# Kernel optimization log

Measured on AMD Instinct MI355X. Metric: run time of the kernel, lower is better.

## Reference

```python
import jax, jax.numpy as jnp
import numpy as np

N, E = 50000, 640000
DIN, DH, DOUT = 128, 256, 128


def _glorot(k, i, o):
    return jax.random.normal(k, (i, o), jnp.float32) / np.sqrt(i)


def setup_inputs() -> dict:
    key = jax.random.key(0)
    ks = jax.random.split(key, 12)
    return {
        "x": jax.random.normal(ks[0], (N, DIN), jnp.float32),
        "edge_index": jax.random.randint(ks[1], (2, E), 0, N, dtype=jnp.int32),
        # SAGEConv 1: in -> hidden (lin_l on aggregated w/ bias, lin_r on root)
        "W1l": _glorot(ks[2], DIN, DH), "b1l": jnp.zeros((DH,), jnp.float32), "W1r": _glorot(ks[3], DIN, DH),
        "g1": jnp.ones((DH,), jnp.float32), "be1": jnp.zeros((DH,), jnp.float32),
        # skip projection (in != hidden)
        "Wsk": _glorot(ks[4], DIN, DH), "bsk": jnp.zeros((DH,), jnp.float32),
        # SAGEConv 2: hidden -> hidden
        "W2l": _glorot(ks[5], DH, DH), "b2l": jnp.zeros((DH,), jnp.float32), "W2r": _glorot(ks[6], DH, DH),
        "g2": jnp.ones((DH,), jnp.float32), "be2": jnp.zeros((DH,), jnp.float32),
        # SAGEConv 3: hidden -> out
        "W3l": _glorot(ks[7], DH, DOUT), "b3l": jnp.zeros((DOUT,), jnp.float32), "W3r": _glorot(ks[8], DH, DOUT),
    }


def _sage_conv(x, src, dst, Wl, bl, Wr, n):
    # mean aggregation of source features into destination nodes
    msg = x[src]                                                 # [E, d]
    agg = jax.ops.segment_sum(msg, dst, num_segments=n)          # [N, d]
    cnt = jax.ops.segment_sum(jnp.ones((src.shape[0],), x.dtype), dst, num_segments=n)
    agg = agg / jnp.maximum(cnt, 1.0)[:, None]
    return agg @ Wl + bl + x @ Wr


def _layernorm(x, g, b):
    mu = jnp.mean(x, axis=-1, keepdims=True)
    var = jnp.mean((x - mu) ** 2, axis=-1, keepdims=True)
    return (x - mu) * jax.lax.rsqrt(var + 1e-5) * g + b


def reference(x, edge_index, W1l, b1l, W1r, g1, be1, Wsk, bsk,
              W2l, b2l, W2r, g2, be2, W3l, b3l, W3r):
    src, dst = edge_index[0], edge_index[1]
    n = x.shape[0]
    # layer 0: conv -> LN -> relu -> (dropout p=0, eval) -> skip via projection
    h = _sage_conv(x, src, dst, W1l, b1l, W1r, n)
    h = jax.nn.relu(_layernorm(h, g1, be1))
    h = h + (x @ Wsk + bsk)
    # layer 1: conv -> LN -> relu -> residual add (shapes match)
    h2 = _sage_conv(h, src, dst, W2l, b2l, W2r, n)
    h2 = jax.nn.relu(_layernorm(h2, g2, be2)) + h
    # final conv (no norm/act)
    return _sage_conv(h2, src, dst, W3l, b3l, W3r, n)
```

## Files before the change

kernel.cpp:

```cpp
#include <hip/hip_runtime.h>


typedef float floatx4 __attribute__((ext_vector_type(4)));
typedef float floatx2 __attribute__((ext_vector_type(2)));
typedef short bf16x8 __attribute__((ext_vector_type(8)));

__device__ inline unsigned short f2bf(float f) {
    unsigned u = __float_as_uint(f);
    unsigned r = (u + 0x7fffu + ((u >> 16) & 1u)) >> 16;
    return (unsigned short)r;
}
__device__ inline float bf2f_lo(unsigned v) { return __uint_as_float(v << 16); }
__device__ inline float bf2f_hi(unsigned v) { return __uint_as_float(v & 0xffff0000u); }

__device__ inline void gl_lds16(const void* g, void* l) {
    __builtin_amdgcn_global_load_lds((const __attribute__((address_space(1))) unsigned int*)g,
                                     (__attribute__((address_space(3))) unsigned int*)l,
                                     16, 0, 0);
}

__global__ void hist_kernel(const int* __restrict__ dst, int* __restrict__ cnt, int E) {
    int i = blockIdx.x * blockDim.x + threadIdx.x;
    if (i < E) atomicAdd(&cnt[dst[i]], 1);
}

#define SCAN_CHUNK 2048

__global__ __launch_bounds__(256) void scan_blocksums(const int* __restrict__ cnt,
                                                      int* __restrict__ bsum, int N) {
    __shared__ int sh[256];
    int t = threadIdx.x;
    int base = blockIdx.x * SCAN_CHUNK + t * 8;
    int s = 0;
#pragma unroll
    for (int i = 0; i < 8; i++) {
        int idx = base + i;
        if (idx < N) s += cnt[idx];
    }
    sh[t] = s;
    __syncthreads();
    for (int off = 1; off < 256; off <<= 1) {
        int v = (t >= off) ? sh[t - off] : 0;
        __syncthreads();
        sh[t] += v;
        __syncthreads();
    }
    if (t == 255) bsum[blockIdx.x] = sh[255];
}

__global__ __launch_bounds__(256) void scan_bsums(const int* __restrict__ bsum,
                                                  int* __restrict__ boff, int NB,
                                                  int* __restrict__ rowptr, int N, int E) {
    __shared__ int sh[256];
    int t = threadIdx.x;
    int v = (t < NB) ? bsum[t] : 0;
    sh[t] = v;
    __syncthreads();
    for (int off = 1; off < 256; off <<= 1) {
        int u = (t >= off) ? sh[t - off] : 0;
        __syncthreads();
        sh[t] += u;
        __syncthreads();
    }
    if (t < NB) boff[t] = sh[t] - v;
    if (t == 0) rowptr[N] = E;
}

__global__ __launch_bounds__(256) void scan_final(const int* __restrict__ cnt,
                                                  const int* __restrict__ boff,
                                                  int* __restrict__ rowptr,
                                                  int* __restrict__ cursor,
                                                  float* __restrict__ invdeg, int N) {
    __shared__ int sh[256];
    int t = threadIdx.x;
    int base = blockIdx.x * SCAN_CHUNK + t * 8;
    int c[8];
    int s = 0;
#pragma unroll
    for (int i = 0; i < 8; i++) {
        int idx = base + i;
        c[i] = (idx < N) ? cnt[idx] : 0;
        s += c[i];
    }
    sh[t] = s;
    __syncthreads();
    for (int off = 1; off < 256; off <<= 1) {
        int v = (t >= off) ? sh[t - off] : 0;
        __syncthreads();
        sh[t] += v;
        __syncthreads();
    }
    int run = boff[blockIdx.x] + sh[t] - s;
#pragma unroll
    for (int i = 0; i < 8; i++) {
        int idx = base + i;
        if (idx < N) {
            rowptr[idx] = run;
            cursor[idx] = run;
            invdeg[idx] = 1.0f / (float)(c[i] > 1 ? c[i] : 1);
            run += c[i];
        }
    }
}

__global__ void scatter_kernel(const int* __restrict__ src, const int* __restrict__ dst,
                               int* __restrict__ cursor, int* __restrict__ col, int E) {
    int i = blockIdx.x * blockDim.x + threadIdx.x;
    if (i < E) {
        int p = atomicAdd(&cursor[dst[i]], 1);
        col[p] = src[i];
    }
}

__global__ void prep_weights(const float* __restrict__ W1l, const float* __restrict__ W1r,
                             const float* __restrict__ Wsk, const float* __restrict__ W2l,
                             const float* __restrict__ W2r, const float* __restrict__ W3l,
                             const float* __restrict__ W3r, const float* __restrict__ b1l,
                             const float* __restrict__ bsk,
                             unsigned short* __restrict__ WtC, unsigned short* __restrict__ Wt2,
                             unsigned short* __restrict__ Wt3, float* __restrict__ biasC) {
    int i = blockIdx.x * blockDim.x + threadIdx.x;
    if (i < 32768) {
        int k = i >> 8, n = i & 255;
        WtC[n * 256 + k] = f2bf(W1l[i]);
    } else if (i < 65536) {
        int j = i - 32768, k = j >> 8, n = j & 255;
        WtC[n * 256 + 128 + k] = f2bf(W1r[j]);
    } else if (i < 98304) {
        int j = i - 65536, k = j >> 8, n = j & 255;
        WtC[(256 + n) * 256 + 128 + k] = f2bf(Wsk[j]);
    } else if (i < 131072) {
        int j = i - 98304, k = j >> 8, n = j & 255;
        WtC[(256 + n) * 256 + k] = 0;
    } else if (i < 196608) {
        int j = i - 131072, k = j >> 8, n = j & 255;
        Wt2[n * 512 + k] = f2bf(W2l[j]);
    } else if (i < 262144) {
        int j = i - 196608, k = j >> 8, n = j & 255;
        Wt2[n * 512 + 256 + k] = f2bf(W2r[j]);
    } else if (i < 294912) {
        int j = i - 262144, k = j >> 7, n = j & 127;
        Wt3[n * 256 + k] = f2bf(W3l[j]);
    } else if (i < 327680) {
        int j = i - 294912, k = j >> 7, n = j & 127;
        Wt3[(128 + n) * 256 + k] = f2bf(W3r[j]);
    } else if (i < 328192) {
        int j = i - 327680;
        biasC[j] = (j < 256) ? b1l[j] : bsk[j - 256];
    }
}

__global__ void cvt_x2(const float* __restrict__ x, unsigned short* __restrict__ A1cat,
                       unsigned char* __restrict__ X8, int total32) {
    int i = blockIdx.x * blockDim.x + threadIdx.x;
    if (i >= total32) return;
    int r = i >> 5, c4 = (i & 31) * 4;
    float4 v = *(const float4*)(x + (size_t)r * 128 + c4);
    ushort4 o;
    o.x = f2bf(v.x); o.y = f2bf(v.y); o.z = f2bf(v.z); o.w = f2bf(v.w);
    *(ushort4*)(A1cat + (size_t)r * 256 + 128 + c4) = o;
    unsigned wpk = 0;
    wpk = __builtin_amdgcn_cvt_pk_fp8_f32(v.x, v.y, wpk, false);
    wpk = __builtin_amdgcn_cvt_pk_fp8_f32(v.z, v.w, wpk, true);
    *(unsigned*)(X8 + (size_t)r * 128 + c4) = wpk;
}

__device__ inline void acc16_fp8(uint4 v, float m, floatx2* a) {
    floatx2 mm = {m, m};
    floatx2 p;
    p = __builtin_amdgcn_cvt_pk_f32_fp8(v.x, false); a[0] = p * mm + a[0];
    p = __builtin_amdgcn_cvt_pk_f32_fp8(v.x, true);  a[1] = p * mm + a[1];
    p = __builtin_amdgcn_cvt_pk_f32_fp8(v.y, false); a[2] = p * mm + a[2];
    p = __builtin_amdgcn_cvt_pk_f32_fp8(v.y, true);  a[3] = p * mm + a[3];
    p = __builtin_amdgcn_cvt_pk_f32_fp8(v.z, false); a[4] = p * mm + a[4];
    p = __builtin_amdgcn_cvt_pk_f32_fp8(v.z, true);  a[5] = p * mm + a[5];
    p = __builtin_amdgcn_cvt_pk_f32_fp8(v.w, false); a[6] = p * mm + a[6];
    p = __builtin_amdgcn_cvt_pk_f32_fp8(v.w, true);  a[7] = p * mm + a[7];
}

__device__ inline void acc8_bf16(uint4 v, float m, floatx2* a) {
    floatx2 mm = {m, m};
    floatx2 p;
    p = (floatx2){bf2f_lo(v.x), bf2f_hi(v.x)}; a[0] = p * mm + a[0];
    p = (floatx2){bf2f_lo(v.y), bf2f_hi(v.y)}; a[1] = p * mm + a[1];
    p = (floatx2){bf2f_lo(v.z), bf2f_hi(v.z)}; a[2] = p * mm + a[2];
    p = (floatx2){bf2f_lo(v.w), bf2f_hi(v.w)}; a[3] = p * mm + a[3];
}

template <int RSB>
__global__ __launch_bounds__(256) void agg_fp8_g(const int* __restrict__ rowptr,
                                                 const int* __restrict__ col,
                                                 const float* __restrict__ invdeg,
                                                 const unsigned char* __restrict__ T8,
                                                 unsigned short* __restrict__ out, int ostride, int N) {
    constexpr int LPR = RSB / 16;
    constexpr int NPW = 64 / LPR;
    int wid = (blockIdx.x * blockDim.x + threadIdx.x) >> 6;
    int lane = threadIdx.x & 63;
    int sub = lane & (LPR - 1);
    int g = lane / LPR;
    int node = wid * NPW + g;
    bool vn = node < N;
    int nc = vn ? node : N - 1;
    int s = rowptr[nc];
    int e = vn ? rowptr[nc + 1] : s;
    const unsigned char* To = T8 + sub * 16;
    floatx2 a[8];
#pragma unroll
    for (int i = 0; i < 8; i++) a[i] = (floatx2){0.f, 0.f};
    for (int j = s; j < e; j += 8) {
        int j1 = (j + 1 < e) ? j + 1 : j;
        int j2 = (j + 2 < e) ? j + 2 : j;
        int j3 = (j + 3 < e) ? j + 3 : j;
        int j4 = (j + 4 < e) ? j + 4 : j;
        int j5 = (j + 5 < e) ? j + 5 : j;
        int j6 = (j + 6 < e) ? j + 6 : j;
        int j7 = (j + 7 < e) ? j + 7 : j;
        float m1 = (j + 1 < e) ? 1.f : 0.f;
        float m2 = (j + 2 < e) ? 1.f : 0.f;
        float m3 = (j + 3 < e) ? 1.f : 0.f;
        float m4 = (j + 4 < e) ? 1.f : 0.f;
        float m5 = (j + 5 < e) ? 1.f : 0.f;
        float m6 = (j + 6 < e) ? 1.f : 0.f;
        float m7 = (j + 7 < e) ? 1.f : 0.f;
        int c0 = col[j], c1 = col[j1], c2 = col[j2], c3 = col[j3];
        int c4 = col[j4], c5 = col[j5], c6 = col[j6], c7 = col[j7];
        uint4 v0 = *(const uint4*)(To + (size_t)c0 * RSB);
        uint4 v1 = *(const uint4*)(To + (size_t)c1 * RSB);
        uint4 v2 = *(const uint4*)(To + (size_t)c2 * RSB);
        uint4 v3 = *(const uint4*)(To + (size_t)c3 * RSB);
        uint4 v4 = *(const uint4*)(To + (size_t)c4 * RSB);
        uint4 v5 = *(const uint4*)(To + (size_t)c5 * RSB);
        uint4 v6 = *(const uint4*)(To + (size_t)c6 * RSB);
        uint4 v7 = *(const uint4*)(To + (size_t)c7 * RSB);
        acc16_fp8(v0, 1.f, a);
        acc16_fp8(v1, m1, a);
        acc16_fp8(v2, m2, a);
        acc16_fp8(v3, m3, a);
        acc16_fp8(v4, m4, a);
        acc16_fp8(v5, m5, a);
        acc16_fp8(v6, m6, a);
        acc16_fp8(v7, m7, a);
    }
    if (vn) {
        float inv = invdeg[node];
        uint4 o1, o2;
        o1.x = (unsigned)f2bf(a[0].x * inv) | ((unsigned)f2bf(a[0].y * inv) << 16);
        o1.y = (unsigned)f2bf(a[1].x * inv) | ((unsigned)f2bf(a[1].y * inv) << 16);
        o1.z = (unsigned)f2bf(a[2].x * inv) | ((unsigned)f2bf(a[2].y * inv) << 16);
        o1.w = (unsigned)f2bf(a[3].x * inv) | ((unsigned)f2bf(a[3].y * inv) << 16);
        o2.x = (unsigned)f2bf(a[4].x * inv) | ((unsigned)f2bf(a[4].y * inv) << 16);
        o2.y = (unsigned)f2bf(a[5].x * inv) | ((unsigned)f2bf(a[5].y * inv) << 16);
        o2.z = (unsigned)f2bf(a[6].x * inv) | ((unsigned)f2bf(a[6].y * inv) << 16);
        o2.w = (unsigned)f2bf(a[7].x * inv) | ((unsigned)f2bf(a[7].y * inv) << 16);
        unsigned short* op = out + (size_t)node * ostride + sub * 16;
        *(uint4*)op = o1;
        *(uint4*)(op + 8) = o2;
    }
}

__global__ __launch_bounds__(256) void agg_fin_g(const int* __restrict__ rowptr,
                                                 const int* __restrict__ col,
                                                 const float* __restrict__ invdeg,
                                                 const unsigned short* __restrict__ T,
                                                 const float* __restrict__ R,
                                                 float* __restrict__ out, int N) {
    int wid = (blockIdx.x * blockDim.x + threadIdx.x) >> 6;
    int lane = threadIdx.x & 63;
    int sub = lane & 15;
    int g = lane >> 4;
    int node = wid * 4 + g;
    bool vn = node < N;
    int nc = vn ? node : N - 1;
    int s = rowptr[nc];
    int e = vn ? rowptr[nc + 1] : s;
    const unsigned short* To = T + sub * 8;
    floatx2 a[4];
#pragma unroll
    for (int i = 0; i < 4; i++) a[i] = (floatx2){0.f, 0.f};
    for (int j = s; j < e; j += 8) {
        int j1 = (j + 1 < e) ? j + 1 : j;
        int j2 = (j + 2 < e) ? j + 2 : j;
        int j3 = (j + 3 < e) ? j + 3 : j;
        int j4 = (j + 4 < e) ? j + 4 : j;
        int j5 = (j + 5 < e) ? j + 5 : j;
        int j6 = (j + 6 < e) ? j + 6 : j;
        int j7 = (j + 7 < e) ? j + 7 : j;
        float m1 = (j + 1 < e) ? 1.f : 0.f;
        float m2 = (j + 2 < e) ? 1.f : 0.f;
        float m3 = (j + 3 < e) ? 1.f : 0.f;
        float m4 = (j + 4 < e) ? 1.f : 0.f;
        float m5 = (j + 5 < e) ? 1.f : 0.f;
        float m6 = (j + 6 < e) ? 1.f : 0.f;
        float m7 = (j + 7 < e) ? 1.f : 0.f;
        int c0 = col[j], c1 = col[j1], c2 = col[j2], c3 = col[j3];
        int c4 = col[j4], c5 = col[j5], c6 = col[j6], c7 = col[j7];
        uint4 v0 = *(const uint4*)(To + (size_t)c0 * 128);
        uint4 v1 = *(const uint4*)(To + (size_t)c1 * 128);
        uint4 v2 = *(const uint4*)(To + (size_t)c2 * 128);
        uint4 v3 = *(const uint4*)(To + (size_t)c3 * 128);
        uint4 v4 = *(const uint4*)(To + (size_t)c4 * 128);
        uint4 v5 = *(const uint4*)(To + (size_t)c5 * 128);
        uint4 v6 = *(const uint4*)(To + (size_t)c6 * 128);
        uint4 v7 = *(const uint4*)(To + (size_t)c7 * 128);
        acc8_bf16(v0, 1.f, a);
        acc8_bf16(v1, m1, a);
        acc8_bf16(v2, m2, a);
        acc8_bf16(v3, m3, a);
        acc8_bf16(v4, m4, a);
        acc8_bf16(v5, m5, a);
        acc8_bf16(v6, m6, a);
        acc8_bf16(v7, m7, a);
    }
    if (vn) {
        float inv = invdeg[node];
        const float* Rp = R + (size_t)node * 128 + sub * 8;
        float4 r1 = *(const float4*)Rp;
        float4 r2 = *(const float4*)(Rp + 4);
        float4 o1, o2;
        o1.x = a[0].x * inv + r1.x; o1.y = a[0].y * inv + r1.y;
        o1.z = a[1].x * inv + r1.z; o1.w = a[1].y * inv + r1.w;
        o2.x = a[2].x * inv + r2.x; o2.y = a[2].y * inv + r2.y;
        o2.z = a[3].x * inv + r2.z; o2.w = a[3].y * inv + r2.w;
        float* op = out + (size_t)node * 128 + sub * 8;
        *(float4*)op = o1;
        *(float4*)(op + 4) = o2;
    }
}

template <int KIT2, int NPAN, int MODE>
__global__ __launch_bounds__(512) void gemm_fused(
    const unsigned short* __restrict__ A, int lda,
    const unsigned short* __restrict__ B, int ldb,
    const float* __restrict__ bias,
    const float* __restrict__ gamma, const float* __restrict__ beta,
    const unsigned short* __restrict__ resid,
    unsigned short* __restrict__ outb,
    unsigned char* __restrict__ h8,
    float* __restrict__ outf, int M) {
    constexpr int COLS = NPAN * 256;
    constexpr int LNW = COLS + 8;
    constexpr int STAGE_E = 128 * 128;
    constexpr int DBUF_F = 2 * STAGE_E / 2;
    constexpr int SMEM_F = (DBUF_F > 32 * LNW) ? DBUF_F : 32 * LNW;
    __shared__ __align__(16) float smemf[SMEM_F];
    unsigned short* sbase = (unsigned short*)smemf;

    int t = threadIdx.x;
    int lane = t & 63, w = t >> 6;
    int bm = blockIdx.x * 128;
    int wm = (w & 1) * 64, wn = (w >> 1) * 64;
    int m16 = lane & 15, kq = lane >> 4;
    const int fsw = m16 & 7;

    floatx4 acc[NPAN][4][4];
#pragma unroll
    for (int p = 0; p < NPAN; p++)
#pragma unroll
        for (int i = 0; i < 4; i++)
#pragma unroll
            for (int j = 0; j < 4; j++) acc[p][i][j] = (floatx4){0.f, 0.f, 0.f, 0.f};

    auto stage = [&](int kt, int bsel) {
        unsigned short* s = sbase + bsel * STAGE_E;
        int k0 = kt * 128;
#pragma unroll
        for (int i = 0; i < 4; i++) {
            int gs = i * 512 + t;
            int kh = gs >> 10;
            int ls = gs & 1023;
            int row = ls >> 3, j = ls & 7;
            int kc = j ^ (row & 7);
            int rowA = bm + row;
            if (rowA > M - 1) rowA = M - 1;
            gl_lds16(A + (size_t)rowA * lda + k0 + kh * 64 + kc * 8, (void*)&s[(size_t)gs * 8]);
        }
    };

    stage(0, 0);
    __syncthreads();
    for (int kt = 0; kt < KIT2; kt++) {
        if (kt + 1 < KIT2) stage(kt + 1, (kt & 1) ^ 1);
        const unsigned short* sA = sbase + (kt & 1) * STAGE_E;
#pragma unroll
        for (int kh = 0; kh < 2; kh++) {
            const unsigned short* sT = sA + kh * 8192;
#pragma unroll
            for (int ks = 0; ks < 2; ks++) {
                int kcl = (ks << 2) | kq;
                bf16x8 af[4];
#pragma unroll
                for (int mi = 0; mi < 4; mi++)
                    af[mi] = *(const bf16x8*)&sT[(wm + mi * 16 + m16) * 64 + ((kcl ^ fsw)) * 8];
#pragma unroll
                for (int p = 0; p < NPAN; p++) {
                    if (MODE == 0 && p == 1 && kt == 0) continue;
                    const unsigned short* Bp = B + (size_t)(wn + p * 256) * ldb + kt * 128 + kh * 64;
                    bf16x8 bf[4];
#pragma unroll
                    for (int ni = 0; ni < 4; ni++)
                        bf[ni] = *(const bf16x8*)&Bp[(size_t)(ni * 16 + m16) * ldb + kcl * 8];
#pragma unroll
                    for (int mi = 0; mi < 4; mi++)
#pragma unroll
                        for (int ni = 0; ni < 4; ni++)
                            acc[p][mi][ni] =
                                __builtin_amdgcn_mfma_f32_16x16x32_bf16(af[mi], bf[ni], acc[p][mi][ni], 0, 0, 0);
                }
            }
        }
        __syncthreads();
    }

    float* lnb = smemf;
    int c4 = lane * 4;
    float4 bu = {0.f, 0.f, 0.f, 0.f}, bs = {0.f, 0.f, 0.f, 0.f};
    float4 gv = {0.f, 0.f, 0.f, 0.f}, bv = {0.f, 0.f, 0.f, 0.f};
    float4 b3 = {0.f, 0.f, 0.f, 0.f};
    if (MODE == 0) {
        bu = *(const float4*)&bias[c4];
        bs = *(const float4*)&bias[256 + c4];
        gv = *(const float4*)&gamma[c4];
        bv = *(const float4*)&beta[c4];
    } else if (MODE == 1) {
        bu = *(const float4*)&bias[c4];
        gv = *(const float4*)&gamma[c4];
        bv = *(const float4*)&beta[c4];
    } else {
        if (lane >= 32) b3 = *(const float4*)&bias[c4 - 128];
    }

#pragma unroll
    for (int g4 = 0; g4 < 4; g4++) {
        if (wm == (g4 >> 1) * 64) {
            int mi0 = (g4 & 1) * 2;
#pragma unroll
            for (int p = 0; p < NPAN; p++)
#pragma unroll
                for (int mm = 0; mm < 2; mm++)
#pragma unroll
                    for (int ni = 0; ni < 4; ni++)
#pragma unroll
                        for (int r = 0; r < 4; r++)
                            lnb[(mm * 16 + kq * 4 + r) * LNW + wn + p * 256 + ni * 16 + m16] =
                                acc[p][mi0 + mm][ni][r];
        }
        __syncthreads();
#pragma unroll
        for (int rr = 0; rr < 4; rr++) {
            int lrow = w * 4 + rr;
            int grow = bm + g4 * 32 + lrow;
            bool valid = grow < M;
            float4 u = *(const float4*)&lnb[lrow * LNW + c4];
            if (MODE <= 1) {
                u.x += bu.x; u.y += bu.y; u.z += bu.z; u.w += bu.w;
                float s1 = (u.x + u.y) + (u.z + u.w);
                float s2 = (u.x * u.x + u.y * u.y) + (u.z * u.z + u.w * u.w);
#pragma unroll
                for (int off = 1; off < 64; off <<= 1) {
                    s1 += __shfl_xor(s1, off, 64);
                    s2 += __shfl_xor(s2, off, 64);
                }
                float mu = s1 * (1.f / 256.f);
                float var = s2 * (1.f / 256.f) - mu * mu;
                float rs = rsqrtf(var + 1e-5f);
                float a0, a1, a2, a3;
                if (MODE == 0) {
                    float4 sv = *(const float4*)&lnb[lrow * LNW + 256 + c4];
                    a0 = sv.x + bs.x; a1 = sv.y + bs.y; a2 = sv.z + bs.z; a3 = sv.w + bs.w;
                } else {
                    int gr = valid ? grow : M - 1;
                    uint2 hv = *(const uint2*)(resid + (size_t)gr * 512 + c4);
                    a0 = bf2f_lo(hv.x); a1 = bf2f_hi(hv.x); a2 = bf2f_lo(hv.y); a3 = bf2f_hi(hv.y);
                }
                float o0 = fmaxf((u.x - mu) * rs * gv.x + bv.x, 0.f) + a0;
                float o1 = fmaxf((u.y - mu) * rs * gv.y + bv.y, 0.f) + a1;
                float o2 = fmaxf((u.z - mu) * rs * gv.z + bv.z, 0.f) + a2;
                float o3 = fmaxf((u.w - mu) * rs * gv.w + bv.w, 0.f) + a3;
                if (valid) {
                    ushort4 o;
                    o.x = f2bf(o0); o.y = f2bf(o1); o.z = f2bf(o2); o.w = f2bf(o3);
                    *(ushort4*)(outb + (size_t)grow * 512 + c4) = o;
                    if (MODE == 0) {
                        unsigned wpk = 0;
                        wpk = __builtin_amdgcn_cvt_pk_fp8_f32(o0, o1, wpk, false);
                        wpk = __builtin_amdgcn_cvt_pk_fp8_f32(o2, o3, wpk, true);
                        *(unsigned*)(h8 + (size_t)grow * 256 + c4) = wpk;
                    }
                }
            } else {
                if (valid) {
                    if (lane < 32) {
                        ushort4 o;
                        o.x = f2bf(u.x); o.y = f2bf(u.y); o.z = f2bf(u.z); o.w = f2bf(u.w);
                        *(ushort4*)(outb + (size_t)grow * 128 + c4) = o;
                    } else {
                        float4 o;
                        o.x = u.x + b3.x; o.y = u.y + b3.y; o.z = u.z + b3.z; o.w = u.w + b3.w;
                        *(float4*)(outf + (size_t)grow * 128 + (c4 - 128)) = o;
                    }
                }
            }
        }
        __syncthreads();
    }
}

extern "C" void kernel_launch(void* const* d_in, const int* in_sizes, int n_in,
                              void* d_out, int out_size, void* d_ws, size_t ws_size,
                              hipStream_t stream) {
    const float* x   = (const float*)d_in[0];
    const int*   ei  = (const int*)d_in[1];
    const float* W1l = (const float*)d_in[2];
    const float* b1l = (const float*)d_in[3];
    const float* W1r = (const float*)d_in[4];
    const float* g1  = (const float*)d_in[5];
    const float* be1 = (const float*)d_in[6];
    const float* Wsk = (const float*)d_in[7];
    const float* bsk = (const float*)d_in[8];
    const float* W2l = (const float*)d_in[9];
    const float* b2l = (const float*)d_in[10];
    const float* W2r = (const float*)d_in[11];
    const float* g2  = (const float*)d_in[12];
    const float* be2 = (const float*)d_in[13];
    const float* W3l = (const float*)d_in[14];
    const float* b3l = (const float*)d_in[15];
    const float* W3r = (const float*)d_in[16];

    const int N = in_sizes[0] / 128;
    const int E = in_sizes[1] / 2;
    const int* src = ei;
    const int* dst = ei + E;

    char* p = (char*)d_ws;
    auto alloc = [&](size_t bytes) {
        void* r = (void*)p;
        p += (bytes + 255) & ~(size_t)255;
        return r;
    };
    int*   cnt    = (int*)alloc(sizeof(int) * N);
    int*   rowptr = (int*)alloc(sizeof(int) * (N + 1));
    int*   cursor = (int*)alloc(sizeof(int) * N);
    float* invdeg = (float*)alloc(sizeof(float) * N);
    int*   col    = (int*)alloc(sizeof(int) * E);
    int*   bsum   = (int*)alloc(sizeof(int) * 256);
    int*   boff   = (int*)alloc(sizeof(int) * 256);
    unsigned short* A1cat = (unsigned short*)alloc(sizeof(short) * (size_t)N * 256);
    unsigned short* A2cat = (unsigned short*)alloc(sizeof(short) * (size_t)N * 512);
    float* r3 = (float*)alloc(sizeof(float) * (size_t)N * 128);
    unsigned char* H8 = (unsigned char*)alloc((size_t)N * 256);
    unsigned char* X8 = (unsigned char*)alloc((size_t)N * 128);
    unsigned short* WtC = (unsigned short*)alloc(sizeof(short) * 512 * 256);
    unsigned short* Wt2 = (unsigned short*)alloc(sizeof(short) * 256 * 512);
    unsigned short* Wt3 = (unsigned short*)alloc(sizeof(short) * 256 * 256);
    float* biasC = (float*)alloc(sizeof(float) * 512);
    unsigned short* t3 = A1cat;

    hipMemsetAsync(cnt, 0, sizeof(int) * N, stream);
    hist_kernel<<<(E + 255) / 256, 256, 0, stream>>>(dst, cnt, E);
    int NB = (N + SCAN_CHUNK - 1) / SCAN_CHUNK;
    scan_blocksums<<<NB, 256, 0, stream>>>(cnt, bsum, N);
    scan_bsums<<<1, 256, 0, stream>>>(bsum, boff, NB, rowptr, N, E);
    scan_final<<<NB, 256, 0, stream>>>(cnt, boff, rowptr, cursor, invdeg, N);
    scatter_kernel<<<(E + 255) / 256, 256, 0, stream>>>(src, dst, cursor, col, E);

    prep_weights<<<(328192 + 255) / 256, 256, 0, stream>>>(W1l, W1r, Wsk, W2l, W2r, W3l, W3r,
                                                           b1l, bsk, WtC, Wt2, Wt3, biasC);
    cvt_x2<<<((N * 32) + 255) / 256, 256, 0, stream>>>(x, A1cat, X8, N * 32);

    int mBlocks = (N + 127) / 128;
    int agg1Blocks = (N + 31) / 32;
    int agg2Blocks = (N + 15) / 16;
    int aggFBlocks = (N + 15) / 16;

    agg_fp8_g<128><<<agg1Blocks, 256, 0, stream>>>(rowptr, col, invdeg, X8, A1cat, 256, N);
    gemm_fused<2, 2, 0><<<mBlocks, 512, 0, stream>>>(A1cat, 256, WtC, 256, biasC, g1, be1,
                                                     nullptr, A2cat + 256, H8, nullptr, N);

    agg_fp8_g<256><<<agg2Blocks, 256, 0, stream>>>(rowptr, col, invdeg, H8, A2cat, 512, N);
    gemm_fused<4, 1, 1><<<mBlocks, 512, 0, stream>>>(A2cat, 512, Wt2, 512, b2l, g2, be2,
                                                     A2cat + 256, A2cat, nullptr, nullptr, N);

    gemm_fused<2, 1, 2><<<mBlocks, 512, 0, stream>>>(A2cat, 512, Wt3, 256, b3l, nullptr, nullptr,
                                                     nullptr, t3, nullptr, r3, N);
    agg_fin_g<<<aggFBlocks, 256, 0, stream>>>(rowptr, col, invdeg, t3, r3, (float*)d_out, N);
}
```

Before: 396.9 us.

## Fuse neighbor aggregation into the per-layer GEMM with LDS-resident operands

Replaces the separate fp8 gather-aggregate kernels for layers 1 and 2 with a fused kernel. Each 128-row block gathers and mean-aggregates neighbor features straight into swizzled LDS tiles, while the root-feature half is loaded asynchronously into LDS. The full-K MFMA GEMM with LayerNorm/ReLU/residual epilogue then runs from those tiles. This removes the global write and re-read of the aggregated bf16 matrix and two kernel launches. In exchange the block needs up to 128KB of LDS, which limits occupancy, and the irregular gather runs in a 512-thread GEMM block with less latency hiding.

```diff
diff --git a/kernel.cpp b/kernel.cpp
--- a/kernel.cpp
+++ b/kernel.cpp
@@ -187,78 +187,6 @@
     p = (floatx2){bf2f_lo(v.w), bf2f_hi(v.w)}; a[3] = p * mm + a[3];
 }
 
-template <int RSB>
-__global__ __launch_bounds__(256) void agg_fp8_g(const int* __restrict__ rowptr,
-                                                 const int* __restrict__ col,
-                                                 const float* __restrict__ invdeg,
-                                                 const unsigned char* __restrict__ T8,
-                                                 unsigned short* __restrict__ out, int ostride, int N) {
-    constexpr int LPR = RSB / 16;
-    constexpr int NPW = 64 / LPR;
-    int wid = (blockIdx.x * blockDim.x + threadIdx.x) >> 6;
-    int lane = threadIdx.x & 63;
-    int sub = lane & (LPR - 1);
-    int g = lane / LPR;
-    int node = wid * NPW + g;
-    bool vn = node < N;
-    int nc = vn ? node : N - 1;
-    int s = rowptr[nc];
-    int e = vn ? rowptr[nc + 1] : s;
-    const unsigned char* To = T8 + sub * 16;
-    floatx2 a[8];
-#pragma unroll
-    for (int i = 0; i < 8; i++) a[i] = (floatx2){0.f, 0.f};
-    for (int j = s; j < e; j += 8) {
-        int j1 = (j + 1 < e) ? j + 1 : j;
-        int j2 = (j + 2 < e) ? j + 2 : j;
-        int j3 = (j + 3 < e) ? j + 3 : j;
-        int j4 = (j + 4 < e) ? j + 4 : j;
-        int j5 = (j + 5 < e) ? j + 5 : j;
-        int j6 = (j + 6 < e) ? j + 6 : j;
-        int j7 = (j + 7 < e) ? j + 7 : j;
-        float m1 = (j + 1 < e) ? 1.f : 0.f;
-        float m2 = (j + 2 < e) ? 1.f : 0.f;
-        float m3 = (j + 3 < e) ? 1.f : 0.f;
-        float m4 = (j + 4 < e) ? 1.f : 0.f;
-        float m5 = (j + 5 < e) ? 1.f : 0.f;
-        float m6 = (j + 6 < e) ? 1.f : 0.f;
-        float m7 = (j + 7 < e) ? 1.f : 0.f;
-        int c0 = col[j], c1 = col[j1], c2 = col[j2], c3 = col[j3];
-        int c4 = col[j4], c5 = col[j5], c6 = col[j6], c7 = col[j7];
-        uint4 v0 = *(const uint4*)(To + (size_t)c0 * RSB);
-        uint4 v1 = *(const uint4*)(To + (size_t)c1 * RSB);
-        uint4 v2 = *(const uint4*)(To + (size_t)c2 * RSB);
-        uint4 v3 = *(const uint4*)(To + (size_t)c3 * RSB);
-        uint4 v4 = *(const uint4*)(To + (size_t)c4 * RSB);
-        uint4 v5 = *(const uint4*)(To + (size_t)c5 * RSB);
-        uint4 v6 = *(const uint4*)(To + (size_t)c6 * RSB);
-        uint4 v7 = *(const uint4*)(To + (size_t)c7 * RSB);
-        acc16_fp8(v0, 1.f, a);
-        acc16_fp8(v1, m1, a);
-        acc16_fp8(v2, m2, a);
-        acc16_fp8(v3, m3, a);
-        acc16_fp8(v4, m4, a);
-        acc16_fp8(v5, m5, a);
-        acc16_fp8(v6, m6, a);
-        acc16_fp8(v7, m7, a);
-    }
-    if (vn) {
-        float inv = invdeg[node];
-        uint4 o1, o2;
-        o1.x = (unsigned)f2bf(a[0].x * inv) | ((unsigned)f2bf(a[0].y * inv) << 16);
-        o1.y = (unsigned)f2bf(a[1].x * inv) | ((unsigned)f2bf(a[1].y * inv) << 16);
-        o1.z = (unsigned)f2bf(a[2].x * inv) | ((unsigned)f2bf(a[2].y * inv) << 16);
-        o1.w = (unsigned)f2bf(a[3].x * inv) | ((unsigned)f2bf(a[3].y * inv) << 16);
-        o2.x = (unsigned)f2bf(a[4].x * inv) | ((unsigned)f2bf(a[4].y * inv) << 16);
-        o2.y = (unsigned)f2bf(a[5].x * inv) | ((unsigned)f2bf(a[5].y * inv) << 16);
-        o2.z = (unsigned)f2bf(a[6].x * inv) | ((unsigned)f2bf(a[6].y * inv) << 16);
-        o2.w = (unsigned)f2bf(a[7].x * inv) | ((unsigned)f2bf(a[7].y * inv) << 16);
-        unsigned short* op = out + (size_t)node * ostride + sub * 16;
-        *(uint4*)op = o1;
-        *(uint4*)(op + 8) = o2;
-    }
-}
-
 __global__ __launch_bounds__(256) void agg_fin_g(const int* __restrict__ rowptr,
                                                  const int* __restrict__ col,
                                                  const float* __restrict__ invdeg,
@@ -328,23 +256,28 @@
     }
 }
 
-template <int KIT2, int NPAN, int MODE>
-__global__ __launch_bounds__(512) void gemm_fused(
-    const unsigned short* __restrict__ A, int lda,
+template <int MODE>
+__global__ __launch_bounds__(512) void fused_layer(
+    const int* __restrict__ rowptr, const int* __restrict__ col,
+    const float* __restrict__ invdeg,
+    const unsigned char* __restrict__ T8, int RSBc,
+    const unsigned short* __restrict__ Aright, int lda,
     const unsigned short* __restrict__ B, int ldb,
     const float* __restrict__ bias,
     const float* __restrict__ gamma, const float* __restrict__ beta,
     const unsigned short* __restrict__ resid,
     unsigned short* __restrict__ outb,
-    unsigned char* __restrict__ h8,
-    float* __restrict__ outf, int M) {
+    unsigned char* __restrict__ h8, int N) {
+    constexpr int KSUB = (MODE == 0) ? 4 : 8;
+    constexpr int GSUB = (MODE == 0) ? 2 : 4;
+    constexpr int RSUB = KSUB - GSUB;
+    constexpr int NPAN = (MODE == 0) ? 2 : 1;
     constexpr int COLS = NPAN * 256;
     constexpr int LNW = COLS + 8;
-    constexpr int STAGE_E = 128 * 128;
-    constexpr int DBUF_F = 2 * STAGE_E / 2;
-    constexpr int SMEM_F = (DBUF_F > 32 * LNW) ? DBUF_F : 32 * LNW;
+    constexpr int A_E = KSUB * 8192;
+    constexpr int SMEM_F = ((A_E / 2) > 32 * LNW) ? (A_E / 2) : 32 * LNW;
     __shared__ __align__(16) float smemf[SMEM_F];
-    unsigned short* sbase = (unsigned short*)smemf;
+    unsigned short* Ab = (unsigned short*)smemf;
 
     int t = threadIdx.x;
     int lane = t & 63, w = t >> 6;
@@ -353,6 +286,94 @@
     int m16 = lane & 15, kq = lane >> 4;
     const int fsw = m16 & 7;
 
+#pragma unroll
+    for (int i = 0; i < RSUB * 2; i++) {
+        int s = i * 512 + t;
+        int st = GSUB + (s >> 10);
+        int ls = s & 1023;
+        int row = ls >> 3, j = ls & 7;
+        int kc = j ^ (row & 7);
+        int rowA = bm + row;
+        if (rowA > N - 1) rowA = N - 1;
+        gl_lds16(Aright + (size_t)rowA * lda + (st - GSUB) * 64 + kc * 8,
+                 (void*)&Ab[(size_t)st * 8192 + (size_t)ls * 8]);
+    }
+
+    {
+        const int LPR = (MODE == 0) ? 8 : 16;
+        const int NG = 512 / LPR;
+        const int NPG = 128 / NG;
+        int sub = t & (LPR - 1);
+        int g = t / LPR;
+        const int RSB = RSBc;
+        const unsigned char* To = T8 + sub * 16;
+#pragma unroll
+        for (int i = 0; i < NPG; i++) {
+            int rl = g + i * NG;
+            int node = bm + rl;
+            bool vn = node < N;
+            int nc = vn ? node : N - 1;
+            int s = rowptr[nc];
+            int e = vn ? rowptr[nc + 1] : s;
+            floatx2 a[8];
+#pragma unroll
+            for (int q = 0; q < 8; q++) a[q] = (floatx2){0.f, 0.f};
+            for (int j = s; j < e; j += 8) {
+                int j1 = (j + 1 < e) ? j + 1 : j;
+                int j2 = (j + 2 < e) ? j + 2 : j;
+                int j3 = (j + 3 < e) ? j + 3 : j;
+                int j4 = (j + 4 < e) ? j + 4 : j;
+                int j5 = (j + 5 < e) ? j + 5 : j;
+                int j6 = (j + 6 < e) ? j + 6 : j;
+                int j7 = (j + 7 < e) ? j + 7 : j;
+                float m1 = (j + 1 < e) ? 1.f : 0.f;
+                float m2 = (j + 2 < e) ? 1.f : 0.f;
+                float m3 = (j + 3 < e) ? 1.f : 0.f;
+                float m4 = (j + 4 < e) ? 1.f : 0.f;
+                float m5 = (j + 5 < e) ? 1.f : 0.f;
+                float m6 = (j + 6 < e) ? 1.f : 0.f;
+                float m7 = (j + 7 < e) ? 1.f : 0.f;
+                int c0 = col[j], c1 = col[j1], c2 = col[j2], c3 = col[j3];
+                int c4 = col[j4], c5 = col[j5], c6 = col[j6], c7 = col[j7];
+                uint4 v0 = *(const uint4*)(To + (size_t)c0 * RSB);
+                uint4 v1 = *(const uint4*)(To + (size_t)c1 * RSB);
+                uint4 v2 = *(const uint4*)(To + (size_t)c2 * RSB);
+                uint4 v3 = *(const uint4*)(To + (size_t)c3 * RSB);
+                uint4 v4 = *(const uint4*)(To + (size_t)c4 * RSB);
+                uint4 v5 = *(const uint4*)(To + (size_t)c5 * RSB);
+                uint4 v6 = *(const uint4*)(To + (size_t)c6 * RSB);
+                uint4 v7 = *(const uint4*)(To + (size_t)c7 * RSB);
+                acc16_fp8(v0, 1.f, a);
+                acc16_fp8(v1, m1, a);
+                acc16_fp8(v2, m2, a);
+                acc16_fp8(v3, m3, a);
+                acc16_fp8(v4, m4, a);
+                acc16_fp8(v5, m5, a);
+                acc16_fp8(v6, m6, a);
+                acc16_fp8(v7, m7, a);
+            }
+            if (vn) {
+                float inv = invdeg[node];
+                uint4 o1, o2;
+                o1.x = (unsigned)f2bf(a[0].x * inv) | ((unsigned)f2bf(a[0].y * inv) << 16);
+                o1.y = (unsigned)f2bf(a[1].x * inv) | ((unsigned)f2bf(a[1].y * inv) << 16);
+                o1.z = (unsigned)f2bf(a[2].x * inv) | ((unsigned)f2bf(a[2].y * inv) << 16);
+                o1.w = (unsigned)f2bf(a[3].x * inv) | ((unsigned)f2bf(a[3].y * inv) << 16);
+                o2.x = (unsigned)f2bf(a[4].x * inv) | ((unsigned)f2bf(a[4].y * inv) << 16);
+                o2.y = (unsigned)f2bf(a[5].x * inv) | ((unsigned)f2bf(a[5].y * inv) << 16);
+                o2.z = (unsigned)f2bf(a[6].x * inv) | ((unsigned)f2bf(a[6].y * inv) << 16);
+                o2.w = (unsigned)f2bf(a[7].x * inv) | ((unsigned)f2bf(a[7].y * inv) << 16);
+                int kt = sub >> 2;
+                int c0k = (sub & 3) * 2;
+                size_t base = (size_t)kt * 8192 + (size_t)rl * 64;
+                *(uint4*)&Ab[base + (size_t)((c0k ^ (rl & 7)) * 8)] = o1;
+                *(uint4*)&Ab[base + (size_t)(((c0k + 1) ^ (rl & 7)) * 8)] = o2;
+            }
+        }
+    }
+    asm volatile("s_waitcnt vmcnt(0)" ::: "memory");
+    __syncthreads();
+
     floatx4 acc[NPAN][4][4];
 #pragma unroll
     for (int p = 0; p < NPAN; p++)
@@ -360,6 +381,139 @@
         for (int i = 0; i < 4; i++)
 #pragma unroll
             for (int j = 0; j < 4; j++) acc[p][i][j] = (floatx4){0.f, 0.f, 0.f, 0.f};
+
+#pragma unroll
+    for (int kt = 0; kt < KSUB; kt++) {
+        const unsigned short* sT = Ab + kt * 8192;
+#pragma unroll
+        for (int ks = 0; ks < 2; ks++) {
+            int kcl = (ks << 2) | kq;
+            bf16x8 af[4];
+#pragma unroll
+            for (int mi = 0; mi < 4; mi++)
+                af[mi] = *(const bf16x8*)&sT[(wm + mi * 16 + m16) * 64 + ((kcl ^ fsw)) * 8];
+#pragma unroll
+            for (int p = 0; p < NPAN; p++) {
+                if (MODE == 0 && p == 1 && kt < 2) continue;
+                const unsigned short* Bp = B + (size_t)(wn + p * 256) * ldb + kt * 64;
+                bf16x8 bf[4];
+#pragma unroll
+                for (int ni = 0; ni < 4; ni++)
+                    bf[ni] = *(const bf16x8*)&Bp[(size_t)(ni * 16 + m16) * ldb + kcl * 8];
+#pragma unroll
+                for (int mi = 0; mi < 4; mi++)
+#pragma unroll
+                    for (int ni = 0; ni < 4; ni++)
+                        acc[p][mi][ni] =
+                            __builtin_amdgcn_mfma_f32_16x16x32_bf16(af[mi], bf[ni], acc[p][mi][ni], 0, 0, 0);
+            }
+        }
+    }
+    __syncthreads();
+
+    float* lnb = smemf;
+    int c4 = lane * 4;
+    float4 bu = {0.f, 0.f, 0.f, 0.f}, bs = {0.f, 0.f, 0.f, 0.f};
+    float4 gv = {0.f, 0.f, 0.f, 0.f}, bv = {0.f, 0.f, 0.f, 0.f};
+    if (MODE == 0) {
+        bu = *(const float4*)&bias[c4];
+        bs = *(const float4*)&bias[256 + c4];
+        gv = *(const float4*)&gamma[c4];
+        bv = *(const float4*)&beta[c4];
+    } else {
+        bu = *(const float4*)&bias[c4];
+        gv = *(const float4*)&gamma[c4];
+        bv = *(const float4*)&beta[c4];
+    }
+
+#pragma unroll
+    for (int g4 = 0; g4 < 4; g4++) {
+        if (wm == (g4 >> 1) * 64) {
+            int mi0 = (g4 & 1) * 2;
+#pragma unroll
+            for (int p = 0; p < NPAN; p++)
+#pragma unroll
+                for (int mm = 0; mm < 2; mm++)
+#pragma unroll
+                    for (int ni = 0; ni < 4; ni++)
+#pragma unroll
+                        for (int r = 0; r < 4; r++)
+                            lnb[(mm * 16 + kq * 4 + r) * LNW + wn + p * 256 + ni * 16 + m16] =
+                                acc[p][mi0 + mm][ni][r];
+        }
+        __syncthreads();
+#pragma unroll
+        for (int rr = 0; rr < 4; rr++) {
+            int lrow = w * 4 + rr;
+            int grow = bm + g4 * 32 + lrow;
+            bool valid = grow < N;
+            float4 u = *(const float4*)&lnb[lrow * LNW + c4];
+            u.x += bu.x; u.y += bu.y; u.z += bu.z; u.w += bu.w;
+            float s1 = (u.x + u.y) + (u.z + u.w);
+            float s2 = (u.x * u.x + u.y * u.y) + (u.z * u.z + u.w * u.w);
+#pragma unroll
+            for (int off = 1; off < 64; off <<= 1) {
+                s1 += __shfl_xor(s1, off, 64);
+                s2 += __shfl_xor(s2, off, 64);
+            }
+            float mu = s1 * (1.f / 256.f);
+            float var = s2 * (1.f / 256.f) - mu * mu;
+            float rs = rsqrtf(var + 1e-5f);
+            float a0, a1, a2, a3;
+            if (MODE == 0) {
+                float4 sv = *(const float4*)&lnb[lrow * LNW + 256 + c4];
+                a0 = sv.x + bs.x; a1 = sv.y + bs.y; a2 = sv.z + bs.z; a3 = sv.w + bs.w;
+            } else {
+                int gr = valid ? grow : N - 1;
+                uint2 hv = *(const uint2*)(resid + (size_t)gr * 512 + c4);
+                a0 = bf2f_lo(hv.x); a1 = bf2f_hi(hv.x); a2 = bf2f_lo(hv.y); a3 = bf2f_hi(hv.y);
+            }
+            float o0 = fmaxf((u.x - mu) * rs * gv.x + bv.x, 0.f) + a0;
+            float o1 = fmaxf((u.y - mu) * rs * gv.y + bv.y, 0.f) + a1;
+            float o2 = fmaxf((u.z - mu) * rs * gv.z + bv.z, 0.f) + a2;
+            float o3 = fmaxf((u.w - mu) * rs * gv.w + bv.w, 0.f) + a3;
+            if (valid) {
+                ushort4 o;
+                o.x = f2bf(o0); o.y = f2bf(o1); o.z = f2bf(o2); o.w = f2bf(o3);
+                *(ushort4*)(outb + (size_t)grow * 512 + c4) = o;
+                if (MODE == 0) {
+                    unsigned wpk = 0;
+                    wpk = __builtin_amdgcn_cvt_pk_fp8_f32(o0, o1, wpk, false);
+                    wpk = __builtin_amdgcn_cvt_pk_fp8_f32(o2, o3, wpk, true);
+                    *(unsigned*)(h8 + (size_t)grow * 256 + c4) = wpk;
+                }
+            }
+        }
+        __syncthreads();
+    }
+}
+
+template <int KIT2>
+__global__ __launch_bounds__(512) void gemm_l3(
+    const unsigned short* __restrict__ A, int lda,
+    const unsigned short* __restrict__ B, int ldb,
+    const float* __restrict__ bias,
+    unsigned short* __restrict__ outb,
+    float* __restrict__ outf, int M) {
+    constexpr int LNW = 256 + 8;
+    constexpr int STAGE_E = 128 * 128;
+    constexpr int DBUF_F = 2 * STAGE_E / 2;
+    constexpr int SMEM_F = (DBUF_F > 32 * LNW) ? DBUF_F : 32 * LNW;
+    __shared__ __align__(16) float smemf[SMEM_F];
+    unsigned short* sbase = (unsigned short*)smemf;
+
+    int t = threadIdx.x;
+    int lane = t & 63, w = t >> 6;
+    int bm = blockIdx.x * 128;
+    int wm = (w & 1) * 64, wn = (w >> 1) * 64;
+    int m16 = lane & 15, kq = lane >> 4;
+    const int fsw = m16 & 7;
+
+    floatx4 acc[4][4];
+#pragma unroll
+    for (int i = 0; i < 4; i++)
+#pragma unroll
+        for (int j = 0; j < 4; j++) acc[i][j] = (floatx4){0.f, 0.f, 0.f, 0.f};
 
     auto stage = [&](int kt, int bsel) {
         unsigned short* s = sbase + bsel * STAGE_E;
@@ -392,21 +546,17 @@
 #pragma unroll
                 for (int mi = 0; mi < 4; mi++)
                     af[mi] = *(const bf16x8*)&sT[(wm + mi * 16 + m16) * 64 + ((kcl ^ fsw)) * 8];
-#pragma unroll
-                for (int p = 0; p < NPAN; p++) {
-                    if (MODE == 0 && p == 1 && kt == 0) continue;
-                    const unsigned short* Bp = B + (size_t)(wn + p * 256) * ldb + kt * 128 + kh * 64;
-                    bf16x8 bf[4];
+                const unsigned short* Bp = B + (size_t)wn * ldb + kt * 128 + kh * 64;
+                bf16x8 bf[4];
+#pragma unroll
+                for (int ni = 0; ni < 4; ni++)
+                    bf[ni] = *(const bf16x8*)&Bp[(size_t)(ni * 16 + m16) * ldb + kcl * 8];
+#pragma unroll
+                for (int mi = 0; mi < 4; mi++)
 #pragma unroll
                     for (int ni = 0; ni < 4; ni++)
-                        bf[ni] = *(const bf16x8*)&Bp[(size_t)(ni * 16 + m16) * ldb + kcl * 8];
-#pragma unroll
-                    for (int mi = 0; mi < 4; mi++)
-#pragma unroll
-                        for (int ni = 0; ni < 4; ni++)
-                            acc[p][mi][ni] =
-                                __builtin_amdgcn_mfma_f32_16x16x32_bf16(af[mi], bf[ni], acc[p][mi][ni], 0, 0, 0);
-                }
+                        acc[mi][ni] =
+                            __builtin_amdgcn_mfma_f32_16x16x32_bf16(af[mi], bf[ni], acc[mi][ni], 0, 0, 0);
             }
         }
         __syncthreads();
@@ -414,36 +564,21 @@
 
     float* lnb = smemf;
     int c4 = lane * 4;
-    float4 bu = {0.f, 0.f, 0.f, 0.f}, bs = {0.f, 0.f, 0.f, 0.f};
-    float4 gv = {0.f, 0.f, 0.f, 0.f}, bv = {0.f, 0.f, 0.f, 0.f};
     float4 b3 = {0.f, 0.f, 0.f, 0.f};
-    if (MODE == 0) {
-        bu = *(const float4*)&bias[c4];
-        bs = *(const float4*)&bias[256 + c4];
-        gv = *(const float4*)&gamma[c4];
-        bv = *(const float4*)&beta[c4];
-    } else if (MODE == 1) {
-        bu = *(const float4*)&bias[c4];
-        gv = *(const float4*)&gamma[c4];
-        bv = *(const float4*)&beta[c4];
-    } else {
-        if (lane >= 32) b3 = *(const float4*)&bias[c4 - 128];
-    }
+    if (lane >= 32) b3 = *(const float4*)&bias[c4 - 128];
 
 #pragma unroll
     for (int g4 = 0; g4 < 4; g4++) {
         if (wm == (g4 >> 1) * 64) {
             int mi0 = (g4 & 1) * 2;
 #pragma unroll
-            for (int p = 0; p < NPAN; p++)
-#pragma unroll
-                for (int mm = 0; mm < 2; mm++)
-#pragma unroll
-                    for (int ni = 0; ni < 4; ni++)
-#pragma unroll
-                        for (int r = 0; r < 4; r++)
-                            lnb[(mm * 16 + kq * 4 + r) * LNW + wn + p * 256 + ni * 16 + m16] =
-                                acc[p][mi0 + mm][ni][r];
+            for (int mm = 0; mm < 2; mm++)
+#pragma unroll
+                for (int ni = 0; ni < 4; ni++)
+#pragma unroll
+                    for (int r = 0; r < 4; r++)
+                        lnb[(mm * 16 + kq * 4 + r) * LNW + wn + ni * 16 + m16] =
+                            acc[mi0 + mm][ni][r];
         }
         __syncthreads();
 #pragma unroll
@@ -452,53 +587,15 @@
             int grow = bm + g4 * 32 + lrow;
             bool valid = grow < M;
             float4 u = *(const float4*)&lnb[lrow * LNW + c4];
-            if (MODE <= 1) {
-                u.x += bu.x; u.y += bu.y; u.z += bu.z; u.w += bu.w;
-                float s1 = (u.x + u.y) + (u.z + u.w);
-                float s2 = (u.x * u.x + u.y * u.y) + (u.z * u.z + u.w * u.w);
-#pragma unroll
-                for (int off = 1; off < 64; off <<= 1) {
-                    s1 += __shfl_xor(s1, off, 64);
-                    s2 += __shfl_xor(s2, off, 64);
-                }
-                float mu = s1 * (1.f / 256.f);
-                float var = s2 * (1.f / 256.f) - mu * mu;
-                float rs = rsqrtf(var + 1e-5f);
-                float a0, a1, a2, a3;
-                if (MODE == 0) {
-                    float4 sv = *(const float4*)&lnb[lrow * LNW + 256 + c4];
-                    a0 = sv.x + bs.x; a1 = sv.y + bs.y; a2 = sv.z + bs.z; a3 = sv.w + bs.w;
+            if (valid) {
+                if (lane < 32) {
+                    ushort4 o;
+                    o.x = f2bf(u.x); o.y = f2bf(u.y); o.z = f2bf(u.z); o.w = f2bf(u.w);
+                    *(ushort4*)(outb + (size_t)grow * 128 + c4) = o;
                 } else {
-                    int gr = valid ? grow : M - 1;
-                    uint2 hv = *(const uint2*)(resid + (size_t)gr * 512 + c4);
-                    a0 = bf2f_lo(hv.x); a1 = bf2f_hi(hv.x); a2 = bf2f_lo(hv.y); a3 = bf2f_hi(hv.y);
-                }
-                float o0 = fmaxf((u.x - mu) * rs * gv.x + bv.x, 0.f) + a0;
-                float o1 = fmaxf((u.y - mu) * rs * gv.y + bv.y, 0.f) + a1;
-                float o2 = fmaxf((u.z - mu) * rs * gv.z + bv.z, 0.f) + a2;
-                float o3 = fmaxf((u.w - mu) * rs * gv.w + bv.w, 0.f) + a3;
-                if (valid) {
-                    ushort4 o;
-                    o.x = f2bf(o0); o.y = f2bf(o1); o.z = f2bf(o2); o.w = f2bf(o3);
-                    *(ushort4*)(outb + (size_t)grow * 512 + c4) = o;
-                    if (MODE == 0) {
-                        unsigned wpk = 0;
-                        wpk = __builtin_amdgcn_cvt_pk_fp8_f32(o0, o1, wpk, false);
-                        wpk = __builtin_amdgcn_cvt_pk_fp8_f32(o2, o3, wpk, true);
-                        *(unsigned*)(h8 + (size_t)grow * 256 + c4) = wpk;
-                    }
-                }
-            } else {
-                if (valid) {
-                    if (lane < 32) {
-                        ushort4 o;
-                        o.x = f2bf(u.x); o.y = f2bf(u.y); o.z = f2bf(u.z); o.w = f2bf(u.w);
-                        *(ushort4*)(outb + (size_t)grow * 128 + c4) = o;
-                    } else {
-                        float4 o;
-                        o.x = u.x + b3.x; o.y = u.y + b3.y; o.z = u.z + b3.z; o.w = u.w + b3.w;
-                        *(float4*)(outf + (size_t)grow * 128 + (c4 - 128)) = o;
-                    }
+                    float4 o;
+                    o.x = u.x + b3.x; o.y = u.y + b3.y; o.z = u.z + b3.z; o.w = u.w + b3.w;
+                    *(float4*)(outf + (size_t)grow * 128 + (c4 - 128)) = o;
                 }
             }
         }
@@ -569,19 +666,18 @@
     cvt_x2<<<((N * 32) + 255) / 256, 256, 0, stream>>>(x, A1cat, X8, N * 32);
 
     int mBlocks = (N + 127) / 128;
-    int agg1Blocks = (N + 31) / 32;
-    int agg2Blocks = (N + 15) / 16;
     int aggFBlocks = (N + 15) / 16;
 
-    agg_fp8_g<128><<<agg1Blocks, 256, 0, stream>>>(rowptr, col, invdeg, X8, A1cat, 256, N);
-    gemm_fused<2, 2, 0><<<mBlocks, 512, 0, stream>>>(A1cat, 256, WtC, 256, biasC, g1, be1,
-                                                     nullptr, A2cat + 256, H8, nullptr, N);
-
-    agg_fp8_g<256><<<agg2Blocks, 256, 0, stream>>>(rowptr, col, invdeg, H8, A2cat, 512, N);
-    gemm_fused<4, 1, 1><<<mBlocks, 512, 0, stream>>>(A2cat, 512, Wt2, 512, b2l, g2, be2,
-                                                     A2cat + 256, A2cat, nullptr, nullptr, N);
-
-    gemm_fused<2, 1, 2><<<mBlocks, 512, 0, stream>>>(A2cat, 512, Wt3, 256, b3l, nullptr, nullptr,
-                                                     nullptr, t3, nullptr, r3, N);
+    fused_layer<0><<<mBlocks, 512, 0, stream>>>(rowptr, col, invdeg, X8, 128,
+                                                A1cat + 128, 256, WtC, 256,
+                                                biasC, g1, be1, nullptr,
+                                                A2cat + 256, H8, N);
+
+    fused_layer<1><<<mBlocks, 512, 0, stream>>>(rowptr, col, invdeg, H8, 256,
+                                                A2cat + 256, 512, Wt2, 512,
+                                                b2l, g2, be2, A2cat + 256,
+                                                A2cat, nullptr, N);
+
+    gemm_l3<2><<<mBlocks, 512, 0, stream>>>(A2cat, 512, Wt3, 256, b3l, t3, r3, N);
     agg_fin_g<<<aggFBlocks, 256, 0, stream>>>(rowptr, col, invdeg, t3, r3, (float*)d_out, N);
 }
```

Result: slower. 407.3 us (+2.6%).
